# Optimization experiments

Hardware: AMD Instinct MI355X
Metric: run time of the kernel (lower is better)

## Reference

```python
import jax, jax.numpy as jnp
import numpy as np
from math import factorial, sqrt, pi

LMAX, NSH = 2, 9
F = 64
N_RBF = 20
N_INTER = 2
N_ATOMS = 1000
N_PAIRS = 10000
CUTOFF = 5.0

# ---------- Clebsch-Gordan coefficients for real spherical harmonics ----------

def _cg_complex(l1, m1, l2, m2, l3, m3):
    # <l1 m1 l2 m2 | l3 m3> via Racah formula
    if m3 != m1 + m2 or not (abs(l1 - l2) <= l3 <= l1 + l2):
        return 0.0
    f = factorial
    pre = sqrt((2 * l3 + 1) * f(l3 + l1 - l2) * f(l3 - l1 + l2) * f(l1 + l2 - l3) / f(l1 + l2 + l3 + 1))
    pre *= sqrt(f(l3 + m3) * f(l3 - m3) * f(l1 - m1) * f(l1 + m1) * f(l2 - m2) * f(l2 + m2))
    s = 0.0
    for k in range(l1 + l2 - l3 + 1):
        d = [k, l1 + l2 - l3 - k, l1 - m1 - k, l2 + m2 - k, l3 - l2 + m1 + k, l3 - l1 - m2 + k]
        if min(d) < 0:
            continue
        s += (-1) ** k / np.prod([float(f(t)) for t in d])
    return pre * s

def _sh_indices(lmax):
    l = np.concatenate([np.full(2 * ll + 1, ll) for ll in range(lmax + 1)])
    m = np.concatenate([np.arange(-ll, ll + 1) for ll in range(lmax + 1)])
    return l, m

def _real_cg(lmax):
    lidx, midx = _sh_indices(lmax)
    n = (lmax + 1) ** 2
    cgc = np.zeros((n, n, n))
    for a in range(n):
        for b in range(n):
            for c in range(n):
                cgc[a, b, c] = _cg_complex(lidx[a], midx[a], lidx[b], midx[b], lidx[c], midx[c])
    # complex -> real spherical harmonic change of basis (per degree l)
    U = np.zeros((n, n), dtype=np.complex128)
    for ll in range(lmax + 1):
        base = ll * ll + ll
        U[base, base] = 1.0
        for m in range(1, ll + 1):
            U[base + m, base - m] = 1 / sqrt(2)
            U[base + m, base + m] = (-1) ** m / sqrt(2)
            U[base - m, base - m] = 1j / sqrt(2)
            U[base - m, base + m] = -1j * (-1) ** m / sqrt(2)
    cgr = np.einsum('ijk,ai,bj,ck->abc', cgc.astype(np.complex128), U, U, U.conj())
    parity = (-1.0) ** lidx
    mask = (parity[:, None, None] * parity[None, :, None]) == parity[None, None, :]
    cgr = np.real(cgr) * mask
    cgr = np.transpose(cgr, (2, 0, 1))  # [s_out, s_in(x), s_filter(Y)]
    s1, s2, s3 = np.nonzero(np.abs(cgr) > 1e-9)
    return s1, s2, s3, cgr[s1, s2, s3].astype(np.float32), lidx

_S1, _S2, _S3, _CGV, _LIDX = _real_cg(LMAX)
IDX1 = jnp.asarray(_S1)            # output sh channel per CG path
IDX2 = jnp.asarray(_S2)            # input-feature sh channel per CG path
IDX3 = jnp.asarray(_S3)            # Ylm sh channel per CG path
CGVAL = jnp.asarray(_CGV)          # CG value per path
WIDX = jnp.asarray(_LIDX[_S3])     # radial-filter degree per CG path
LIDX = jnp.asarray(_LIDX)          # degree of each of the 9 sh channels

# ---------- real spherical harmonics (lmax=2, orthonormal, m=-l..l order) ----------

def _rsh(u):
    x, y, z = u[:, 0], u[:, 1], u[:, 2]
    c1 = sqrt(3.0 / (4.0 * pi))
    c2 = 0.5 * sqrt(15.0 / pi)
    return jnp.stack([
        jnp.full_like(x, 0.5 / sqrt(pi)),
        c1 * y, c1 * z, c1 * x,
        c2 * x * y,
        c2 * y * z,
        0.25 * sqrt(5.0 / pi) * (3.0 * z * z - 1.0),
        c2 * x * z,
        0.25 * sqrt(15.0 / pi) * (x * x - y * y),
    ], axis=1)


def setup_inputs() -> dict:
    key = jax.random.key(0)
    ks = jax.random.split(key, 10)
    atomic_numbers = jax.random.randint(ks[0], (N_ATOMS,), 0, 100)
    r_ij = 1.5 * jax.random.normal(ks[1], (N_PAIRS, 3), dtype=jnp.float32)
    idx_i = jnp.sort(jax.random.randint(ks[2], (N_PAIRS,), 0, N_ATOMS))
    idx_j = jax.random.randint(ks[3], (N_PAIRS,), 0, N_ATOMS)
    emb = jax.random.normal(ks[4], (100, F), dtype=jnp.float32)
    def s(k, sh, fan):
        return jax.random.normal(k, sh, dtype=jnp.float32) / float(np.sqrt(fan))
    Wf = s(ks[5], (N_INTER, N_RBF, (LMAX + 1) * F), N_RBF)
    bf = jnp.zeros((N_INTER, (LMAX + 1) * F), jnp.float32)
    W1 = s(ks[6], (N_INTER, F, F), F)
    W2 = s(ks[7], (N_INTER, F, F), F)
    W3 = s(ks[8], (N_INTER, F, F), F)
    Wg = s(ks[9], (N_INTER, F, (LMAX + 1) * F), F)
    bg = jnp.zeros((N_INTER, (LMAX + 1) * F), jnp.float32)
    return dict(atomic_numbers=atomic_numbers, r_ij=r_ij, idx_i=idx_i, idx_j=idx_j,
                emb=emb, Wf=Wf, bf=bf, W1=W1, W2=W2, W3=W3, Wg=Wg, bg=bg)


def reference(atomic_numbers, r_ij, idx_i, idx_j, emb, Wf, bf, W1, W2, W3, Wg, bg):
    n_atoms = atomic_numbers.shape[0]
    d = jnp.linalg.norm(r_ij, axis=1, keepdims=True)          # [P,1]
    Yij = _rsh(r_ij / d)                                       # [P,9]
    offsets = jnp.linspace(0.0, CUTOFF, N_RBF)                 # GaussianRBF
    width = CUTOFF / (N_RBF - 1)
    radial = jnp.exp((-0.5 / (width * width)) * (d - offsets) ** 2)   # [P,n_rbf]
    cut = 0.5 * (jnp.cos(d * (pi / CUTOFF)) + 1.0) * (d < CUTOFF)     # [P,1]
    # nuclear embedding + scalar2rsh (zero-pad l>0 channels)
    x = jnp.zeros((n_atoms, NSH, F), emb.dtype).at[:, 0, :].set(emb[atomic_numbers])
    for t in range(N_INTER):
        # SO3Convolution
        Wij = (radial @ Wf[t] + bf[t]).reshape(-1, LMAX + 1, F) * cut[:, :, None]  # [P,lmax+1,F]
        xj = x[idx_j]                                                              # [P,9,F]
        v = xj[:, IDX2] * Yij[:, IDX3, None] * Wij[:, WIDX] * CGVAL[None, :, None]  # [P,nnz,F]
        yij = jnp.zeros_like(xj).at[:, IDX1].add(v)                                 # CG scatter
        dx = jax.ops.segment_sum(yij, idx_i, num_segments=n_atoms)                  # edge->node scatter
        # mixing1 + SO3TensorProduct
        ddx = dx @ W1[t]
        tp = jnp.zeros_like(dx).at[:, IDX1].add(dx[:, IDX2] * ddx[:, IDX3] * CGVAL[None, :, None])
        dx = (dx + tp) @ W2[t]
        # SO3ParametricGatedNonlinearity (gate from l=0 channel)
        gate = (dx[:, 0] @ Wg[t] + bg[t]).reshape(-1, LMAX + 1, F)
        dx = dx * jax.nn.sigmoid(gate[:, LIDX])
        dx = dx @ W3[t]
        x = x + dx
    return x  # multipole_representation [n_atoms, 9, F]; x[:,0] is scalar_representation
```

## Files before the change

kernel.cpp:

```cpp
#include <hip/hip_runtime.h>
#include <cmath>

constexpr int kNsh    = 9;
constexpr int kF      = 64;
constexpr int kNrbf   = 20;
constexpr int kNAtoms = 1000;
constexpr int kNPairs = 10000;
constexpr float kCutoffF = 5.0f;
constexpr int kMaxNZ  = 200;
constexpr int kCp     = 12;
constexpr int kXs     = kF * kCp;

struct CGSparse {
  int n;
  int c[kMaxNZ];
  int a[kMaxNZ];
  int b[kMaxNZ];
  float v[kMaxNZ];
};

constexpr double cfact(int n) {
  double r = 1.0;
  for (int i = 2; i <= n; i++) r *= (double)i;
  return r;
}
constexpr double cabs_(double x) { return x < 0 ? -x : x; }
constexpr double csqrt_(double x) {
  if (x <= 0.0) return 0.0;
  double g = x < 1.0 ? 1.0 : x;
  for (int i = 0; i < 60; i++) g = 0.5 * (g + x / g);
  return g;
}

constexpr double cg_cplx(int l1, int m1, int l2, int m2, int l3, int m3) {
  if (m3 != m1 + m2) return 0.0;
  int lo = l1 > l2 ? l1 - l2 : l2 - l1;
  if (l3 < lo || l3 > l1 + l2) return 0.0;
  double pre = csqrt_((2 * l3 + 1) * cfact(l3 + l1 - l2) * cfact(l3 - l1 + l2) *
                      cfact(l1 + l2 - l3) / cfact(l1 + l2 + l3 + 1));
  pre *= csqrt_(cfact(l3 + m3) * cfact(l3 - m3) * cfact(l1 - m1) *
                cfact(l1 + m1) * cfact(l2 - m2) * cfact(l2 + m2));
  double s = 0.0;
  for (int k = 0; k <= l1 + l2 - l3; k++) {
    int d0 = k, d1 = l1 + l2 - l3 - k, d2 = l1 - m1 - k;
    int d3 = l2 + m2 - k, d4 = l3 - l2 + m1 + k, d5 = l3 - l1 - m2 + k;
    if (d0 < 0 || d1 < 0 || d2 < 0 || d3 < 0 || d4 < 0 || d5 < 0) continue;
    double den = cfact(d0) * cfact(d1) * cfact(d2) * cfact(d3) * cfact(d4) * cfact(d5);
    s += ((k % 2) ? -1.0 : 1.0) / den;
  }
  return pre * s;
}

constexpr CGSparse build_cg() {
  CGSparse out{};
  int lidx[9] = {0, 1, 1, 1, 2, 2, 2, 2, 2};
  int midx[9] = {0, -1, 0, 1, -2, -1, 0, 1, 2};
  double Ur[9][9] = {};
  double Ui[9][9] = {};
  for (int l = 0; l <= 2; l++) {
    int base = l * l + l;
    Ur[base][base] = 1.0;
    for (int m = 1; m <= l; m++) {
      double s2 = 1.0 / csqrt_(2.0);
      double sgn = (m % 2) ? -1.0 : 1.0;
      Ur[base + m][base - m] = s2;
      Ur[base + m][base + m] = sgn * s2;
      Ui[base - m][base - m] = s2;
      Ui[base - m][base + m] = -sgn * s2;
    }
  }
  double cgr[9][9][9] = {};
  for (int i = 0; i < 9; i++)
    for (int j = 0; j < 9; j++)
      for (int k = 0; k < 9; k++) {
        double cv = cg_cplx(lidx[i], midx[i], lidx[j], midx[j], lidx[k], midx[k]);
        if (cv == 0.0) continue;
        for (int a2 = 0; a2 < 9; a2++) {
          if (Ur[a2][i] == 0.0 && Ui[a2][i] == 0.0) continue;
          for (int b2 = 0; b2 < 9; b2++) {
            if (Ur[b2][j] == 0.0 && Ui[b2][j] == 0.0) continue;
            for (int c2 = 0; c2 < 9; c2++) {
              if (Ur[c2][k] == 0.0 && Ui[c2][k] == 0.0) continue;
              double ar = Ur[a2][i], ai = Ui[a2][i];
              double br = Ur[b2][j], bi = Ui[b2][j];
              double cr = Ur[c2][k], ci = -Ui[c2][k];
              double pr = ar * br - ai * bi;
              double pi = ar * bi + ai * br;
              double rr = pr * cr - pi * ci;
              cgr[c2][a2][b2] += rr * cv;
            }
          }
        }
      }
  int n = 0;
  for (int c2 = 0; c2 < 9; c2++)
    for (int a2 = 0; a2 < 9; a2++)
      for (int b2 = 0; b2 < 9; b2++) {
        bool mask = ((lidx[a2] + lidx[b2]) % 2) == (lidx[c2] % 2);
        double v = mask ? cgr[c2][a2][b2] : 0.0;
        if (cabs_(v) > 1e-9) {
          out.c[n] = c2;
          out.a[n] = a2;
          out.b[n] = b2;
          out.v[n] = (float)v;
          n++;
        }
      }
  out.n = n;
  return out;
}

constexpr CGSparse CG = build_cg();
static_assert(CG.n > 0 && CG.n <= kMaxNZ, "CG table size out of range");

constexpr int kPreBlkPairs = kNPairs / 4;
constexpr int kPreBlkInit  = kNAtoms * kF / 256;
constexpr int kPreBlkSeg   = (kNAtoms + 1 + 255) / 256;
constexpr int kPreBlkTotal = kPreBlkPairs + kPreBlkInit + kPreBlkSeg;

__global__ __launch_bounds__(256) void k_pre(
    const float* __restrict__ rij, const float* __restrict__ Wf,
    const float* __restrict__ bf, const int* __restrict__ Z,
    const float* __restrict__ emb, const int* __restrict__ idx_i,
    float* __restrict__ Ypd, float* __restrict__ Wpair,
    float* __restrict__ x0, int* __restrict__ seg) {
  const int blk = blockIdx.x;
  if (blk < kPreBlkPairs) {
    int wv = threadIdx.x >> 6;
    int f = threadIdx.x & 63;
    int p = blk * 4 + wv;
    float rx = rij[3 * p + 0], ry = rij[3 * p + 1], rz = rij[3 * p + 2];
    float d = sqrtf(rx * rx + ry * ry + rz * rz);
    float inv = 1.0f / d;
    float x = rx * inv, y = ry * inv, z = rz * inv;
    const float c0 = 0.28209479177387814f;
    const float c1 = 0.4886025119029199f;
    const float c2 = 1.0925484305920792f;
    const float c3 = 0.31539156525252005f;
    const float c4 = 0.5462742152960396f;
    if (f < 9) {
      float yv =
          (f == 0) ? c0 :
          (f == 1) ? c1 * y :
          (f == 2) ? c1 * z :
          (f == 3) ? c1 * x :
          (f == 4) ? c2 * x * y :
          (f == 5) ? c2 * y * z :
          (f == 6) ? c3 * (3.0f * z * z - 1.0f) :
          (f == 7) ? c2 * x * z :
                     c4 * (x * x - y * y);
      Ypd[p * 16 + f] = yv;
    }
    float cut = (d < kCutoffF) ? 0.5f * (cosf(d * (float)(M_PI / 5.0)) + 1.0f) : 0.0f;
    float radial[kNrbf];
    const float width = kCutoffF / (kNrbf - 1);
    const float coef = -0.5f / (width * width);
    #pragma unroll
    for (int k = 0; k < kNrbf; k++) {
      float off = (kCutoffF * k) / (kNrbf - 1);
      float tt = d - off;
      radial[k] = expf(coef * tt * tt);
    }
    #pragma unroll
    for (int t = 0; t < 2; t++) {
      #pragma unroll
      for (int l = 0; l < 3; l++) {
        float w = bf[t * 192 + l * 64 + f];
        #pragma unroll
        for (int k = 0; k < kNrbf; k++) {
          w += radial[k] * Wf[t * (kNrbf * 192) + k * 192 + l * 64 + f];
        }
        Wpair[t * (kNPairs * 192) + p * 192 + l * 64 + f] = w * cut;
      }
    }
  } else if (blk < kPreBlkPairs + kPreBlkInit) {
    int tid = (blk - kPreBlkPairs) * 256 + threadIdx.x;
    int atom = tid >> 6;
    int f = tid & 63;
    float e = emb[Z[atom] * kF + f];
    float4* b = (float4*)(x0 + atom * kXs + f * kCp);
    b[0] = make_float4(e, 0.f, 0.f, 0.f);
    b[1] = make_float4(0.f, 0.f, 0.f, 0.f);
    b[2] = make_float4(0.f, 0.f, 0.f, 0.f);
  } else {
    int a = (blk - kPreBlkPairs - kPreBlkInit) * 256 + threadIdx.x;
    if (a <= kNAtoms) {
      int lo = 0, hi = kNPairs;
      while (lo < hi) {
        int mid = (lo + hi) >> 1;
        if (idx_i[mid] < a) lo = mid + 1; else hi = mid;
      }
      seg[a] = lo;
    }
  }
}

__global__ __launch_bounds__(256) void k_message(
    const float* __restrict__ x_in, const int* __restrict__ idx_j,
    const float* __restrict__ Ypd, const float* __restrict__ Wpair,
    float* __restrict__ ypair) {
  const int wv = threadIdx.x >> 6;
  const int f = threadIdx.x & 63;
  const int p = blockIdx.x * 4 + wv;
  const float* Yp = Ypd + p * 16;
  const float* Wp = Wpair + p * 192;
  float Wl0 = Wp[f], Wl1 = Wp[64 + f], Wl2 = Wp[128 + f];
  const int j = __builtin_amdgcn_readfirstlane(idx_j[p]);
  const float* xj = x_in + j * kXs + f * kCp;
  float xv[12];
  *(float4*)&xv[0] = *(const float4*)(xj + 0);
  *(float4*)&xv[4] = *(const float4*)(xj + 4);
  *(float4*)&xv[8] = *(const float4*)(xj + 8);
  float YW[9];
  YW[0] = Yp[0] * Wl0;
  YW[1] = Yp[1] * Wl1;
  YW[2] = Yp[2] * Wl1;
  YW[3] = Yp[3] * Wl1;
  #pragma unroll
  for (int b = 4; b < 9; b++) YW[b] = Yp[b] * Wl2;
  float y[12] = {0, 0, 0, 0, 0, 0, 0, 0, 0, 0, 0, 0};
  #pragma unroll
  for (int e = 0; e < CG.n; e++) {
    y[CG.c[e]] += CG.v[e] * YW[CG.b[e]] * xv[CG.a[e]];
  }
  float* yp = ypair + p * kXs + f * kCp;
  *(float4*)(yp + 0) = *(float4*)&y[0];
  *(float4*)(yp + 4) = *(float4*)&y[4];
  *(float4*)(yp + 8) = *(float4*)&y[8];
}

__device__ __forceinline__ void stage_w(const float* __restrict__ W,
                                        float* __restrict__ sW, int tid) {
  const float4* g4 = (const float4*)W;
  float4* s4 = (float4*)sW;
  #pragma unroll
  for (int r = 0; r < 4; r++) s4[r * 256 + tid] = g4[r * 256 + tid];
}

__device__ __forceinline__ void mm_phase(const float* __restrict__ sA,
                                         const float* __restrict__ sW,
                                         float* __restrict__ sRw,
                                         int k0, int cg, int fb) {
  if (cg >= 3) return;
  const int c0 = cg * 4;
  float acc[4][4];
  #pragma unroll
  for (int i = 0; i < 4; i++)
    #pragma unroll
    for (int j = 0; j < 4; j++) acc[i][j] = 0.f;
  #pragma unroll 4
  for (int kk = 0; kk < 16; kk++) {
    int k = k0 + kk;
    float4 av = *(const float4*)(sA + k * kCp + c0);
    float4 wv = *(const float4*)(sW + k * kF + fb);
    float a[4] = {av.x, av.y, av.z, av.w};
    float w[4] = {wv.x, wv.y, wv.z, wv.w};
    #pragma unroll
    for (int i = 0; i < 4; i++)
      #pragma unroll
      for (int j = 0; j < 4; j++) acc[i][j] += a[i] * w[j];
  }
  #pragma unroll
  for (int j = 0; j < 4; j++) {
    float4 v = {acc[0][j], acc[1][j], acc[2][j], acc[3][j]};
    *(float4*)(sRw + (fb + j) * kCp + c0) = v;
  }
}

template <int FINAL>
__global__ __launch_bounds__(256) void k_update(
    const float* __restrict__ ypair, const int* __restrict__ seg,
    const float* __restrict__ x_in, const float* __restrict__ W1,
    const float* __restrict__ W2, const float* __restrict__ W3,
    const float* __restrict__ Wg, const float* __restrict__ bg,
    float* __restrict__ x_out) {
  const int atom = blockIdx.x;
  const int tid = threadIdx.x;
  const int wv = tid >> 6;
  const int lane = tid & 63;
  const int cg = lane >> 4;
  const int fg = lane & 15;
  const int fb = fg * 4;
  const int k0 = wv * 16;

  __shared__ __align__(16) float sA[kF * kCp];
  __shared__ __align__(16) float sW[kF * kF];
  __shared__ __align__(16) float sR[4][kF * kCp];
  __shared__ __align__(16) float sGp[4][192];

  stage_w(W1, sW, tid);

  {
    float4 a0 = {0, 0, 0, 0}, a1 = {0, 0, 0, 0}, a2 = {0, 0, 0, 0};
    const int s0 = seg[atom], s1 = seg[atom + 1];
    #pragma unroll 2
    for (int p = s0 + wv; p < s1; p += 4) {
      const float4* yp = (const float4*)(ypair + p * kXs + lane * kCp);
      float4 v0 = yp[0], v1 = yp[1], v2 = yp[2];
      a0.x += v0.x; a0.y += v0.y; a0.z += v0.z; a0.w += v0.w;
      a1.x += v1.x; a1.y += v1.y; a1.z += v1.z; a1.w += v1.w;
      a2.x += v2.x; a2.y += v2.y; a2.z += v2.z; a2.w += v2.w;
    }
    float4* r4 = (float4*)(sR[wv] + lane * kCp);
    r4[0] = a0; r4[1] = a1; r4[2] = a2;
  }
  __syncthreads();
  {
    const int i = tid * 3;
    #pragma unroll
    for (int d = 0; d < 3; d++) {
      sA[i + d] = sR[0][i + d] + sR[1][i + d] + sR[2][i + d] + sR[3][i + d];
    }
  }
  __syncthreads();

  mm_phase(sA, sW, sR[wv], k0, cg, fb);
  __syncthreads();

  stage_w(W2, sW, tid);
  if (wv == 0) {
    float dxv[12], ddx[12];
    {
      const float4* sa = (const float4*)(sA + lane * kCp);
      *(float4*)&dxv[0] = sa[0]; *(float4*)&dxv[4] = sa[1]; *(float4*)&dxv[8] = sa[2];
    }
    #pragma unroll
    for (int c = 0; c < 12; c++) {
      ddx[c] = sR[0][lane * kCp + c] + sR[1][lane * kCp + c] +
               sR[2][lane * kCp + c] + sR[3][lane * kCp + c];
    }
    float t2[12];
    #pragma unroll
    for (int c = 0; c < 9; c++) t2[c] = dxv[c];
    t2[9] = 0.f; t2[10] = 0.f; t2[11] = 0.f;
    #pragma unroll
    for (int e = 0; e < CG.n; e++) {
      t2[CG.c[e]] += CG.v[e] * dxv[CG.a[e]] * ddx[CG.b[e]];
    }
    float4* sa = (float4*)(sA + lane * kCp);
    sa[0] = *(float4*)&t2[0]; sa[1] = *(float4*)&t2[4]; sa[2] = *(float4*)&t2[8];
  }
  __syncthreads();

  mm_phase(sA, sW, sR[wv], k0, cg, fb);
  __syncthreads();

  stage_w(W3, sW, tid);
  {
    float g0 = 0.f, g1 = 0.f, g2 = 0.f;
    #pragma unroll 4
    for (int kk = 0; kk < 16; kk++) {
      int k = k0 + kk;
      float a = sR[0][k * kCp] + sR[1][k * kCp] + sR[2][k * kCp] + sR[3][k * kCp];
      g0 += a * Wg[k * 192 + lane];
      g1 += a * Wg[k * 192 + 64 + lane];
      g2 += a * Wg[k * 192 + 128 + lane];
    }
    sGp[wv][lane] = g0;
    sGp[wv][64 + lane] = g1;
    sGp[wv][128 + lane] = g2;
  }
  __syncthreads();

  if (wv == 0) {
    float dx2v[12];
    #pragma unroll
    for (int c = 0; c < 12; c++) {
      dx2v[c] = sR[0][lane * kCp + c] + sR[1][lane * kCp + c] +
                sR[2][lane * kCp + c] + sR[3][lane * kCp + c];
    }
    float g0 = bg[lane] + sGp[0][lane] + sGp[1][lane] + sGp[2][lane] + sGp[3][lane];
    float g1 = bg[64 + lane] + sGp[0][64 + lane] + sGp[1][64 + lane] +
               sGp[2][64 + lane] + sGp[3][64 + lane];
    float g2 = bg[128 + lane] + sGp[0][128 + lane] + sGp[1][128 + lane] +
               sGp[2][128 + lane] + sGp[3][128 + lane];
    g0 = 1.f / (1.f + expf(-g0));
    g1 = 1.f / (1.f + expf(-g1));
    g2 = 1.f / (1.f + expf(-g2));
    float dx3[12];
    dx3[0] = dx2v[0] * g0;
    dx3[1] = dx2v[1] * g1;
    dx3[2] = dx2v[2] * g1;
    dx3[3] = dx2v[3] * g1;
    #pragma unroll
    for (int c = 4; c < 9; c++) dx3[c] = dx2v[c] * g2;
    dx3[9] = 0.f; dx3[10] = 0.f; dx3[11] = 0.f;
    float4* sa = (float4*)(sA + lane * kCp);
    sa[0] = *(float4*)&dx3[0]; sa[1] = *(float4*)&dx3[4]; sa[2] = *(float4*)&dx3[8];
  }
  __syncthreads();

  mm_phase(sA, sW, sR[wv], k0, cg, fb);
  __syncthreads();

  if (FINAL == 0) {
    const int i = tid * 3;
    #pragma unroll
    for (int d = 0; d < 3; d++) {
      float v = sR[0][i + d] + sR[1][i + d] + sR[2][i + d] + sR[3][i + d] +
                x_in[atom * kXs + i + d];
      x_out[atom * kXs + i + d] = v;
    }
  } else {
    for (int i = tid; i < kNsh * kF; i += 256) {
      int c = i >> 6, f = i & 63;
      int o = f * kCp + c;
      float v = sR[0][o] + sR[1][o] + sR[2][o] + sR[3][o] +
                x_in[atom * kXs + o];
      x_out[atom * (kNsh * kF) + i] = v;
    }
  }
}

extern "C" void kernel_launch(void* const* d_in, const int* in_sizes, int n_in,
                              void* d_out, int out_size, void* d_ws, size_t ws_size,
                              hipStream_t stream) {
  const int* Z        = (const int*)d_in[0];
  const float* rij    = (const float*)d_in[1];
  const int* idx_i    = (const int*)d_in[2];
  const int* idx_j    = (const int*)d_in[3];
  const float* emb    = (const float*)d_in[4];
  const float* Wf     = (const float*)d_in[5];
  const float* bf     = (const float*)d_in[6];
  const float* W1     = (const float*)d_in[7];
  const float* W2     = (const float*)d_in[8];
  const float* W3     = (const float*)d_in[9];
  const float* Wg     = (const float*)d_in[10];
  const float* bg     = (const float*)d_in[11];
  float* x_final = (float*)d_out;

  float* x0    = (float*)d_ws;
  float* x1    = x0 + kNAtoms * kXs;
  float* Ypd   = x1 + kNAtoms * kXs;
  float* Wpair = Ypd + kNPairs * 16;
  float* ypair = Wpair + 2 * kNPairs * 192;
  int*   seg   = (int*)(ypair + kNPairs * kXs);

  k_pre<<<kPreBlkTotal, 256, 0, stream>>>(
      rij, Wf, bf, Z, emb, idx_i, Ypd, Wpair, x0, seg);

  k_message<<<kNPairs / 4, 256, 0, stream>>>(x0, idx_j, Ypd, Wpair, ypair);
  k_update<0><<<kNAtoms, 256, 0, stream>>>(
      ypair, seg, x0, W1, W2, W3, Wg, bg, x1);

  k_message<<<kNPairs / 4, 256, 0, stream>>>(
      x1, idx_j, Ypd, Wpair + kNPairs * 192, ypair);
  k_update<1><<<kNAtoms, 256, 0, stream>>>(
      ypair, seg, x1, W1 + kF * kF, W2 + kF * kF, W3 + kF * kF,
      Wg + kF * 192, bg + 192, x_final);
}
```

Before: 152.8 us.

## Fuse message computation into per-atom update kernel and drop x0 initialization

```diff
diff --git a/kernel.cpp b/kernel.cpp
--- a/kernel.cpp
+++ b/kernel.cpp
@@ -114,16 +114,14 @@
 static_assert(CG.n > 0 && CG.n <= kMaxNZ, "CG table size out of range");
 
 constexpr int kPreBlkPairs = kNPairs / 4;
-constexpr int kPreBlkInit  = kNAtoms * kF / 256;
 constexpr int kPreBlkSeg   = (kNAtoms + 1 + 255) / 256;
-constexpr int kPreBlkTotal = kPreBlkPairs + kPreBlkInit + kPreBlkSeg;
+constexpr int kPreBlkTotal = kPreBlkPairs + kPreBlkSeg;
 
 __global__ __launch_bounds__(256) void k_pre(
     const float* __restrict__ rij, const float* __restrict__ Wf,
-    const float* __restrict__ bf, const int* __restrict__ Z,
-    const float* __restrict__ emb, const int* __restrict__ idx_i,
+    const float* __restrict__ bf, const int* __restrict__ idx_i,
     float* __restrict__ Ypd, float* __restrict__ Wpair,
-    float* __restrict__ x0, int* __restrict__ seg) {
+    int* __restrict__ seg) {
   const int blk = blockIdx.x;
   if (blk < kPreBlkPairs) {
     int wv = threadIdx.x >> 6;
@@ -173,17 +171,8 @@
         Wpair[t * (kNPairs * 192) + p * 192 + l * 64 + f] = w * cut;
       }
     }
-  } else if (blk < kPreBlkPairs + kPreBlkInit) {
-    int tid = (blk - kPreBlkPairs) * 256 + threadIdx.x;
-    int atom = tid >> 6;
-    int f = tid & 63;
-    float e = emb[Z[atom] * kF + f];
-    float4* b = (float4*)(x0 + atom * kXs + f * kCp);
-    b[0] = make_float4(e, 0.f, 0.f, 0.f);
-    b[1] = make_float4(0.f, 0.f, 0.f, 0.f);
-    b[2] = make_float4(0.f, 0.f, 0.f, 0.f);
   } else {
-    int a = (blk - kPreBlkPairs - kPreBlkInit) * 256 + threadIdx.x;
+    int a = (blk - kPreBlkPairs) * 256 + threadIdx.x;
     if (a <= kNAtoms) {
       int lo = 0, hi = kNPairs;
       while (lo < hi) {
@@ -195,40 +184,6 @@
   }
 }
 
-__global__ __launch_bounds__(256) void k_message(
-    const float* __restrict__ x_in, const int* __restrict__ idx_j,
-    const float* __restrict__ Ypd, const float* __restrict__ Wpair,
-    float* __restrict__ ypair) {
-  const int wv = threadIdx.x >> 6;
-  const int f = threadIdx.x & 63;
-  const int p = blockIdx.x * 4 + wv;
-  const float* Yp = Ypd + p * 16;
-  const float* Wp = Wpair + p * 192;
-  float Wl0 = Wp[f], Wl1 = Wp[64 + f], Wl2 = Wp[128 + f];
-  const int j = __builtin_amdgcn_readfirstlane(idx_j[p]);
-  const float* xj = x_in + j * kXs + f * kCp;
-  float xv[12];
-  *(float4*)&xv[0] = *(const float4*)(xj + 0);
-  *(float4*)&xv[4] = *(const float4*)(xj + 4);
-  *(float4*)&xv[8] = *(const float4*)(xj + 8);
-  float YW[9];
-  YW[0] = Yp[0] * Wl0;
-  YW[1] = Yp[1] * Wl1;
-  YW[2] = Yp[2] * Wl1;
-  YW[3] = Yp[3] * Wl1;
-  #pragma unroll
-  for (int b = 4; b < 9; b++) YW[b] = Yp[b] * Wl2;
-  float y[12] = {0, 0, 0, 0, 0, 0, 0, 0, 0, 0, 0, 0};
-  #pragma unroll
-  for (int e = 0; e < CG.n; e++) {
-    y[CG.c[e]] += CG.v[e] * YW[CG.b[e]] * xv[CG.a[e]];
-  }
-  float* yp = ypair + p * kXs + f * kCp;
-  *(float4*)(yp + 0) = *(float4*)&y[0];
-  *(float4*)(yp + 4) = *(float4*)&y[4];
-  *(float4*)(yp + 8) = *(float4*)&y[8];
-}
-
 __device__ __forceinline__ void stage_w(const float* __restrict__ W,
                                         float* __restrict__ sW, int tid) {
   const float4* g4 = (const float4*)W;
@@ -240,9 +195,9 @@
 __device__ __forceinline__ void mm_phase(const float* __restrict__ sA,
                                          const float* __restrict__ sW,
                                          float* __restrict__ sRw,
-                                         int k0, int cg, int fb) {
-  if (cg >= 3) return;
-  const int c0 = cg * 4;
+                                         int k0, int cgi, int fb) {
+  if (cgi >= 3) return;
+  const int c0 = cgi * 4;
   float acc[4][4];
   #pragma unroll
   for (int i = 0; i < 4; i++)
@@ -267,9 +222,11 @@
   }
 }
 
-template <int FINAL>
-__global__ __launch_bounds__(256) void k_update(
-    const float* __restrict__ ypair, const int* __restrict__ seg,
+template <int T>
+__global__ __launch_bounds__(256) void k_inter(
+    const float* __restrict__ Ypd, const float* __restrict__ Wpt,
+    const int* __restrict__ seg, const int* __restrict__ idx_j,
+    const int* __restrict__ Z, const float* __restrict__ emb,
     const float* __restrict__ x_in, const float* __restrict__ W1,
     const float* __restrict__ W2, const float* __restrict__ W3,
     const float* __restrict__ Wg, const float* __restrict__ bg,
@@ -278,9 +235,8 @@
   const int tid = threadIdx.x;
   const int wv = tid >> 6;
   const int lane = tid & 63;
-  const int cg = lane >> 4;
-  const int fg = lane & 15;
-  const int fb = fg * 4;
+  const int cgi = lane >> 4;
+  const int fb = (lane & 15) * 4;
   const int k0 = wv * 16;
 
   __shared__ __align__(16) float sA[kF * kCp];
@@ -291,18 +247,45 @@
   stage_w(W1, sW, tid);
 
   {
-    float4 a0 = {0, 0, 0, 0}, a1 = {0, 0, 0, 0}, a2 = {0, 0, 0, 0};
+    float y[12];
+    #pragma unroll
+    for (int c = 0; c < 12; c++) y[c] = 0.f;
     const int s0 = seg[atom], s1 = seg[atom + 1];
-    #pragma unroll 2
-    for (int p = s0 + wv; p < s1; p += 4) {
-      const float4* yp = (const float4*)(ypair + p * kXs + lane * kCp);
-      float4 v0 = yp[0], v1 = yp[1], v2 = yp[2];
-      a0.x += v0.x; a0.y += v0.y; a0.z += v0.z; a0.w += v0.w;
-      a1.x += v1.x; a1.y += v1.y; a1.z += v1.z; a1.w += v1.w;
-      a2.x += v2.x; a2.y += v2.y; a2.z += v2.z; a2.w += v2.w;
+    for (int p0 = s0 + wv; p0 < s1; p0 += 4) {
+      const int p = __builtin_amdgcn_readfirstlane(p0);
+      const int j = __builtin_amdgcn_readfirstlane(idx_j[p]);
+      const float* Wp = Wpt + p * 192;
+      float Wl0 = Wp[lane], Wl1 = Wp[64 + lane], Wl2 = Wp[128 + lane];
+      const float* Yp = Ypd + p * 16;
+      float YW[9];
+      YW[0] = Yp[0] * Wl0;
+      YW[1] = Yp[1] * Wl1;
+      YW[2] = Yp[2] * Wl1;
+      YW[3] = Yp[3] * Wl1;
+      #pragma unroll
+      for (int b = 4; b < 9; b++) YW[b] = Yp[b] * Wl2;
+      if (T == 0) {
+        float e = emb[Z[j] * kF + lane];
+        #pragma unroll
+        for (int q = 0; q < CG.n; q++) {
+          if (CG.a[q] == 0) y[CG.c[q]] += CG.v[q] * YW[CG.b[q]] * e;
+        }
+      } else {
+        const float* xj = x_in + j * kXs + lane * kCp;
+        float xv[12];
+        *(float4*)&xv[0] = *(const float4*)(xj + 0);
+        *(float4*)&xv[4] = *(const float4*)(xj + 4);
+        *(float4*)&xv[8] = *(const float4*)(xj + 8);
+        #pragma unroll
+        for (int q = 0; q < CG.n; q++) {
+          y[CG.c[q]] += CG.v[q] * YW[CG.b[q]] * xv[CG.a[q]];
+        }
+      }
     }
     float4* r4 = (float4*)(sR[wv] + lane * kCp);
-    r4[0] = a0; r4[1] = a1; r4[2] = a2;
+    r4[0] = *(float4*)&y[0];
+    r4[1] = *(float4*)&y[4];
+    r4[2] = *(float4*)&y[8];
   }
   __syncthreads();
   {
@@ -314,7 +297,7 @@
   }
   __syncthreads();
 
-  mm_phase(sA, sW, sR[wv], k0, cg, fb);
+  mm_phase(sA, sW, sR[wv], k0, cgi, fb);
   __syncthreads();
 
   stage_w(W2, sW, tid);
@@ -322,7 +305,9 @@
     float dxv[12], ddx[12];
     {
       const float4* sa = (const float4*)(sA + lane * kCp);
-      *(float4*)&dxv[0] = sa[0]; *(float4*)&dxv[4] = sa[1]; *(float4*)&dxv[8] = sa[2];
+      *(float4*)&dxv[0] = sa[0];
+      *(float4*)&dxv[4] = sa[1];
+      *(float4*)&dxv[8] = sa[2];
     }
     #pragma unroll
     for (int c = 0; c < 12; c++) {
@@ -334,15 +319,17 @@
     for (int c = 0; c < 9; c++) t2[c] = dxv[c];
     t2[9] = 0.f; t2[10] = 0.f; t2[11] = 0.f;
     #pragma unroll
-    for (int e = 0; e < CG.n; e++) {
-      t2[CG.c[e]] += CG.v[e] * dxv[CG.a[e]] * ddx[CG.b[e]];
+    for (int q = 0; q < CG.n; q++) {
+      t2[CG.c[q]] += CG.v[q] * dxv[CG.a[q]] * ddx[CG.b[q]];
     }
     float4* sa = (float4*)(sA + lane * kCp);
-    sa[0] = *(float4*)&t2[0]; sa[1] = *(float4*)&t2[4]; sa[2] = *(float4*)&t2[8];
-  }
-  __syncthreads();
-
-  mm_phase(sA, sW, sR[wv], k0, cg, fb);
+    sa[0] = *(float4*)&t2[0];
+    sa[1] = *(float4*)&t2[4];
+    sa[2] = *(float4*)&t2[8];
+  }
+  __syncthreads();
+
+  mm_phase(sA, sW, sR[wv], k0, cgi, fb);
   __syncthreads();
 
   stage_w(W3, sW, tid);
@@ -386,20 +373,25 @@
     for (int c = 4; c < 9; c++) dx3[c] = dx2v[c] * g2;
     dx3[9] = 0.f; dx3[10] = 0.f; dx3[11] = 0.f;
     float4* sa = (float4*)(sA + lane * kCp);
-    sa[0] = *(float4*)&dx3[0]; sa[1] = *(float4*)&dx3[4]; sa[2] = *(float4*)&dx3[8];
-  }
-  __syncthreads();
-
-  mm_phase(sA, sW, sR[wv], k0, cg, fb);
-  __syncthreads();
-
-  if (FINAL == 0) {
+    sa[0] = *(float4*)&dx3[0];
+    sa[1] = *(float4*)&dx3[4];
+    sa[2] = *(float4*)&dx3[8];
+  }
+  __syncthreads();
+
+  mm_phase(sA, sW, sR[wv], k0, cgi, fb);
+  __syncthreads();
+
+  if (T == 0) {
+    const int zi = Z[atom];
     const int i = tid * 3;
     #pragma unroll
     for (int d = 0; d < 3; d++) {
-      float v = sR[0][i + d] + sR[1][i + d] + sR[2][i + d] + sR[3][i + d] +
-                x_in[atom * kXs + i + d];
-      x_out[atom * kXs + i + d] = v;
+      const int idx = i + d;
+      const int c = idx % kCp;
+      float v = sR[0][idx] + sR[1][idx] + sR[2][idx] + sR[3][idx];
+      if (c == 0) v += emb[zi * kF + idx / kCp];
+      x_out[atom * kXs + idx] = v;
     }
   } else {
     for (int i = tid; i < kNsh * kF; i += 256) {
@@ -427,25 +419,21 @@
   const float* W3     = (const float*)d_in[9];
   const float* Wg     = (const float*)d_in[10];
   const float* bg     = (const float*)d_in[11];
-  float* x_final = (float*)d_out;
-
-  float* x0    = (float*)d_ws;
-  float* x1    = x0 + kNAtoms * kXs;
+  float* out = (float*)d_out;
+
+  float* x1    = (float*)d_ws;
   float* Ypd   = x1 + kNAtoms * kXs;
   float* Wpair = Ypd + kNPairs * 16;
-  float* ypair = Wpair + 2 * kNPairs * 192;
-  int*   seg   = (int*)(ypair + kNPairs * kXs);
-
-  k_pre<<<kPreBlkTotal, 256, 0, stream>>>(
-      rij, Wf, bf, Z, emb, idx_i, Ypd, Wpair, x0, seg);
-
-  k_message<<<kNPairs / 4, 256, 0, stream>>>(x0, idx_j, Ypd, Wpair, ypair);
-  k_update<0><<<kNAtoms, 256, 0, stream>>>(
-      ypair, seg, x0, W1, W2, W3, Wg, bg, x1);
-
-  k_message<<<kNPairs / 4, 256, 0, stream>>>(
-      x1, idx_j, Ypd, Wpair + kNPairs * 192, ypair);
-  k_update<1><<<kNAtoms, 256, 0, stream>>>(
-      ypair, seg, x1, W1 + kF * kF, W2 + kF * kF, W3 + kF * kF,
-      Wg + kF * 192, bg + 192, x_final);
-}
+  int*   seg   = (int*)(Wpair + 2 * kNPairs * 192);
+
+  k_pre<<<kPreBlkTotal, 256, 0, stream>>>(rij, Wf, bf, idx_i, Ypd, Wpair, seg);
+
+  k_inter<0><<<kNAtoms, 256, 0, stream>>>(
+      Ypd, Wpair, seg, idx_j, Z, emb, x1,
+      W1, W2, W3, Wg, bg, x1);
+
+  k_inter<1><<<kNAtoms, 256, 0, stream>>>(
+      Ypd, Wpair + kNPairs * 192, seg, idx_j, Z, emb, x1,
+      W1 + kF * kF, W2 + kF * kF, W3 + kF * kF,
+      Wg + kF * 192, bg + 192, out);
+}
```

New measurement: 126.6 us. 1.21x faster.
